# Kernel optimization log

Measured on AMD Instinct MI355X. Metric: run time of the kernel, lower is better.

The kernel has to match this reference:

```python
import jax, jax.numpy as jnp
import numpy as np

B, S, L, H, N_ITEMS = 16, 20, 64, 768, 50000  # sessions, max items/session, tokens/item, hidden, catalog
T = S * L
TEMP = 0.05       # config.temp
PAD_POS = 50      # pad item position id (see torch code)
EPS = 1e-8        # torch CosineSimilarity eps


def setup_inputs() -> dict:
    key = jax.random.key(0)
    k1, k2, k3, k4 = jax.random.split(key, 4)
    hidden = jax.random.normal(k1, (B, T, H), jnp.float32)
    emb = jax.random.normal(k2, (N_ITEMS, H), jnp.float32)
    # item position ids: each item's L tokens share position 1..S; padded items -> 50
    pos = np.tile(np.repeat(np.arange(1, S + 1), L)[None, :], (B, 1))  # [B,T]
    sess_len = np.asarray(jax.random.randint(k3, (B,), S // 2, S + 1))  # items per session
    item_idx = np.repeat(np.arange(S), L)[None, :]                      # [1,T]
    pos = np.where(item_idx < sess_len[:, None], pos, PAD_POS).astype(np.int32)
    attn = (pos != PAD_POS).astype(np.int32)
    attrs = np.asarray(jax.random.randint(k4, (B, T), 0, 4)).astype(np.int32)
    return {
        "hidden_states": hidden,
        "item_embedding": emb,
        "attention_mask": jnp.asarray(attn),
        "item_position_ids": jnp.asarray(pos),
        "attr_type_ids": jnp.asarray(attrs),
    }


def reference(hidden_states, item_embedding, attention_mask, item_position_ids, attr_type_ids):
    # --- RecformerPooler (pooler_type='item'): nan-mean pool tokens per item ---
    item_ids = jnp.arange(1, S + 1, dtype=item_position_ids.dtype)
    mask = item_position_ids[:, None, :] == item_ids[None, :, None]      # [B,S,T]
    counts = mask.sum(-1)                                                # [B,S]
    valid = counts > 0                                                   # items present in session
    maskf = mask.astype(hidden_states.dtype)
    pooled = jnp.einsum('bst,bth->bsh', maskf, hidden_states)
    pooled = pooled / jnp.maximum(counts, 1)[..., None].astype(hidden_states.dtype)
    # (torch produces NaN rows for invalid items; we carry `valid` instead)

    # --- Similarity: cosine / temp vs full item catalog ---
    pn = jnp.maximum(jnp.linalg.norm(pooled, axis=-1, keepdims=True), EPS)
    en = jnp.maximum(jnp.linalg.norm(item_embedding, axis=-1, keepdims=True), EPS)
    sim = jnp.einsum('bsh,nh->bns', pooled / pn, item_embedding / en) / TEMP  # [B,N,S]

    # --- reduce_session('maxsim'): NaN -> -inf, max over session items ---
    sim = jnp.where(valid[:, None, :], sim, -jnp.inf)
    scores = sim.max(axis=-1)  # [B, N]; trailing mean over attr dim (size 1) is identity
    return scores
```

## Files before the change

### kernel.cpp

```cpp
#include <hip/hip_runtime.h>

#define B_ 16
#define S_ 20
#define L_ 64
#define T_ 1280
#define H_ 768
#define NITEMS 50000
#define TEMP 0.05f
#define EPSN 1e-8f

#define BM 320
#define BN 128
#define BK 32
#define NKT (H_ / BK)

typedef __attribute__((ext_vector_type(8))) short short8;
typedef __attribute__((ext_vector_type(4))) short short4v;
typedef __attribute__((ext_vector_type(4))) float f32x4;

__device__ __forceinline__ unsigned short f2bf(float f) {
    unsigned int u = __float_as_uint(f);
    u = u + 0x7FFFu + ((u >> 16) & 1u);
    return (unsigned short)(u >> 16);
}

typedef __attribute__((address_space(3))) void lds_void;
typedef const __attribute__((address_space(1))) void gbl_void;
__device__ __forceinline__ void load_lds16(const void* g, void* l) {
    __builtin_amdgcn_global_load_lds((gbl_void*)g, (lds_void*)l, 16, 0, 0);
}

__global__ __launch_bounds__(192) void pool_kernel(const float* __restrict__ hidden,
                                                   const int* __restrict__ pos,
                                                   unsigned short* __restrict__ A,
                                                   int* __restrict__ valid) {
    const int row = blockIdx.x;
    const int b = row / S_, s = row % S_;
    const int tid = threadIdx.x;

    __shared__ float wgt[L_];
    __shared__ int cntS;
    __shared__ float red[3];

    const int* pbase = pos + b * T_ + s * L_;
    if (tid < L_) {
        const int match = (pbase[tid] == s + 1) ? 1 : 0;
        unsigned long long bal = __ballot(match);
        wgt[tid] = match ? 1.0f : 0.0f;
        if (tid == 0) cntS = (int)__popcll(bal);
    }
    __syncthreads();

    const int cnt = cntS;
    const float inv = 1.0f / (float)(cnt > 0 ? cnt : 1);
    const float* hbase = hidden + ((size_t)b * T_ + (size_t)s * L_) * H_ + tid * 4;

    float a0 = 0.f, a1 = 0.f, a2 = 0.f, a3 = 0.f;
#pragma unroll 8
    for (int t = 0; t < L_; ++t) {
        const float w = wgt[t];
        const float4 v = *reinterpret_cast<const float4*>(hbase + (size_t)t * H_);
        a0 += w * v.x; a1 += w * v.y; a2 += w * v.z; a3 += w * v.w;
    }
    a0 *= inv; a1 *= inv; a2 *= inv; a3 *= inv;

    float ss = a0 * a0 + a1 * a1 + a2 * a2 + a3 * a3;
#pragma unroll
    for (int off = 32; off; off >>= 1) ss += __shfl_xor(ss, off, 64);
    const int wave = tid >> 6, lane = tid & 63;
    if (lane == 0) red[wave] = ss;
    __syncthreads();
    const float tot = red[0] + red[1] + red[2];
    const float scale = 1.0f / (fmaxf(sqrtf(tot), EPSN) * TEMP);

    short4v w4;
    w4[0] = (short)f2bf(a0 * scale);
    w4[1] = (short)f2bf(a1 * scale);
    w4[2] = (short)f2bf(a2 * scale);
    w4[3] = (short)f2bf(a3 * scale);
    const int slot = tid >> 1;
    const int slotSw = (slot & ~3) | ((slot & 3) ^ (row & 3));
    *reinterpret_cast<short4v*>(A + (size_t)row * H_ + slotSw * 8 + (tid & 1) * 4) = w4;
    if (tid == 0) valid[row] = (cnt > 0) ? 1 : 0;
}

__global__ __launch_bounds__(256, 2) void gemm_kernel(const float* __restrict__ emb,
                                                      const unsigned short* __restrict__ A,
                                                      const int* __restrict__ valid,
                                                      float* __restrict__ out) {
    const int n0 = blockIdx.x * BN;
    const int tid = threadIdx.x;
    const int wave = tid >> 6, lane = tid & 63, quad = lane >> 4, lq = lane & 15;

    __shared__ alignas(16) short As[2][BM * BK];
    __shared__ alignas(16) short Bs[2][BN * BK];
    __shared__ float sEn[BN];
    __shared__ int sMask[B_];

    if (tid < B_) {
        int m = 0;
        for (int s = 0; s < S_; ++s) m |= (valid[tid * S_ + s] ? 1 : 0) << s;
        sMask[tid] = m;
    }

    const unsigned short* aSrc = A + (size_t)(tid >> 2) * H_ + (tid & 3) * 8;
    const int brLoc = tid >> 1;
    int brGlb = n0 + brLoc;
    if (brGlb > NITEMS - 1) brGlb = NITEMS - 1;
    const float* bSrc = emb + (size_t)brGlb * H_ + (tid & 1) * 16;
    const int bw0 = brLoc * BK + ((((tid & 1) * 2) + 0) ^ (brLoc & 3)) * 8;
    const int bw1 = brLoc * BK + ((((tid & 1) * 2) + 1) ^ (brLoc & 3)) * 8;

    float rowSq = 0.f;

    {
        const float4 v0 = *reinterpret_cast<const float4*>(bSrc);
        const float4 v1 = *reinterpret_cast<const float4*>(bSrc + 4);
        const float4 v2 = *reinterpret_cast<const float4*>(bSrc + 8);
        const float4 v3 = *reinterpret_cast<const float4*>(bSrc + 12);
#pragma unroll
        for (int i = 0; i < 5; ++i)
            load_lds16(aSrc + i * 64 * H_, (char*)(&As[0][0]) + tid * 16 + i * 4096);
        rowSq += v0.x * v0.x + v0.y * v0.y + v0.z * v0.z + v0.w * v0.w;
        rowSq += v1.x * v1.x + v1.y * v1.y + v1.z * v1.z + v1.w * v1.w;
        rowSq += v2.x * v2.x + v2.y * v2.y + v2.z * v2.z + v2.w * v2.w;
        rowSq += v3.x * v3.x + v3.y * v3.y + v3.z * v3.z + v3.w * v3.w;
        short8 lo, hi;
        lo[0] = (short)f2bf(v0.x); lo[1] = (short)f2bf(v0.y);
        lo[2] = (short)f2bf(v0.z); lo[3] = (short)f2bf(v0.w);
        lo[4] = (short)f2bf(v1.x); lo[5] = (short)f2bf(v1.y);
        lo[6] = (short)f2bf(v1.z); lo[7] = (short)f2bf(v1.w);
        hi[0] = (short)f2bf(v2.x); hi[1] = (short)f2bf(v2.y);
        hi[2] = (short)f2bf(v2.z); hi[3] = (short)f2bf(v2.w);
        hi[4] = (short)f2bf(v3.x); hi[5] = (short)f2bf(v3.y);
        hi[6] = (short)f2bf(v3.z); hi[7] = (short)f2bf(v3.w);
        *reinterpret_cast<short8*>(&Bs[0][bw0]) = lo;
        *reinterpret_cast<short8*>(&Bs[0][bw1]) = hi;
    }

    f32x4 acc[5][8];
#pragma unroll
    for (int i = 0; i < 5; ++i)
#pragma unroll
        for (int j = 0; j < 8; ++j) acc[i][j] = (f32x4)0.f;

    __syncthreads();

    int cur = 0;
    for (int kt = 0; kt < NKT; ++kt) {
        float4 v0, v1, v2, v3;
        const bool more = (kt + 1 < NKT);
        if (more) {
            const int k0 = (kt + 1) * BK;
            v0 = *reinterpret_cast<const float4*>(bSrc + k0);
            v1 = *reinterpret_cast<const float4*>(bSrc + k0 + 4);
            v2 = *reinterpret_cast<const float4*>(bSrc + k0 + 8);
            v3 = *reinterpret_cast<const float4*>(bSrc + k0 + 12);
#pragma unroll
            for (int i = 0; i < 5; ++i)
                load_lds16(aSrc + k0 + i * 64 * H_,
                           (char*)(&As[cur ^ 1][0]) + tid * 16 + i * 4096);
        }

        short8 bF[8];
#pragma unroll
        for (int nf = 0; nf < 8; ++nf) {
            const int rB = nf * 16 + lq;
            bF[nf] = *reinterpret_cast<const short8*>(
                &Bs[cur][rB * BK + ((quad ^ (lq & 3)) * 8)]);
        }

#pragma unroll
        for (int mf = 0; mf < 5; ++mf) {
            const int rA = wave * 80 + mf * 16 + lq;
            const short8 aF = *reinterpret_cast<const short8*>(
                &As[cur][rA * BK + ((quad ^ (lq & 3)) * 8)]);
#pragma unroll
            for (int nf = 0; nf < 8; ++nf)
                acc[mf][nf] =
                    __builtin_amdgcn_mfma_f32_16x16x32_bf16(aF, bF[nf], acc[mf][nf], 0, 0, 0);
        }

        if (more) {
            rowSq += v0.x * v0.x + v0.y * v0.y + v0.z * v0.z + v0.w * v0.w;
            rowSq += v1.x * v1.x + v1.y * v1.y + v1.z * v1.z + v1.w * v1.w;
            rowSq += v2.x * v2.x + v2.y * v2.y + v2.z * v2.z + v2.w * v2.w;
            rowSq += v3.x * v3.x + v3.y * v3.y + v3.z * v3.z + v3.w * v3.w;
            short8 lo, hi;
            lo[0] = (short)f2bf(v0.x); lo[1] = (short)f2bf(v0.y);
            lo[2] = (short)f2bf(v0.z); lo[3] = (short)f2bf(v0.w);
            lo[4] = (short)f2bf(v1.x); lo[5] = (short)f2bf(v1.y);
            lo[6] = (short)f2bf(v1.z); lo[7] = (short)f2bf(v1.w);
            hi[0] = (short)f2bf(v2.x); hi[1] = (short)f2bf(v2.y);
            hi[2] = (short)f2bf(v2.z); hi[3] = (short)f2bf(v2.w);
            hi[4] = (short)f2bf(v3.x); hi[5] = (short)f2bf(v3.y);
            hi[6] = (short)f2bf(v3.z); hi[7] = (short)f2bf(v3.w);
            *reinterpret_cast<short8*>(&Bs[cur ^ 1][bw0]) = lo;
            *reinterpret_cast<short8*>(&Bs[cur ^ 1][bw1]) = hi;
        }
        __syncthreads();
        cur ^= 1;
    }

    rowSq += __shfl_xor(rowSq, 1, 64);
    if (!(tid & 1)) sEn[brLoc] = fmaxf(sqrtf(rowSq), EPSN);
    __syncthreads();

#pragma unroll
    for (int nf = 0; nf < 8; ++nf) {
        const int ncol = nf * 16 + lq;
        const int n = n0 + ncol;
        const float inv_en = 1.0f / sEn[ncol];
#pragma unroll
        for (int bl = 0; bl < 4; ++bl) {
            const int bb = wave * 4 + bl;
            const int msk = sMask[bb];
            const int rLo = bl * S_;
            float lm = -__builtin_inff();
            const int mfLo = rLo >> 4;
            const int mfHi = (rLo + S_ - 1) >> 4;
#pragma unroll
            for (int mf = mfLo; mf <= mfHi; ++mf)
#pragma unroll
                for (int e = 0; e < 4; ++e) {
                    const int r = mf * 16 + quad * 4 + e;
                    const unsigned off = (unsigned)(r - rLo);
                    const bool ok = (off < (unsigned)S_) && ((msk >> off) & 1);
                    lm = ok ? fmaxf(lm, acc[mf][nf][e]) : lm;
                }
            lm = fmaxf(lm, __shfl_xor(lm, 16, 64));
            lm = fmaxf(lm, __shfl_xor(lm, 32, 64));
            if (quad == 0 && n < NITEMS)
                out[(size_t)bb * NITEMS + n] = lm * inv_en;
        }
    }
}

extern "C" void kernel_launch(void* const* d_in, const int* in_sizes, int n_in,
                              void* d_out, int out_size, void* d_ws, size_t ws_size,
                              hipStream_t stream) {
    const float* hidden = (const float*)d_in[0];
    const float* emb    = (const float*)d_in[1];
    const int*   pos    = (const int*)d_in[3];
    float* out = (float*)d_out;

    unsigned short* Abf = (unsigned short*)d_ws;
    int* valid = (int*)((char*)d_ws + (size_t)320 * 768 * 2);

    pool_kernel<<<dim3(320), dim3(192), 0, stream>>>(hidden, pos, Abf, valid);
    gemm_kernel<<<dim3((NITEMS + BN - 1) / BN), dim3(256), 0, stream>>>(emb, Abf, valid, out);
}
```

Before: 295.5 us.

## Rework GEMM LDS swizzle, move barrier before async loads, widen pool kernel

The GEMM main loop now uses one barrier per K-step, placed before the async global-to-LDS A loads are issued, with explicit vmcnt waits in place of the trailing __syncthreads. This aims to overlap the next tile's loads with the MFMA work and cut barrier stalls. The LDS XOR swizzle changes from row&3 to (row>>1)&3 for both A and B, with matching changes to the pool kernel's output layout, to reduce bank conflicts for the 16-lane fragment reads. The pool kernel moves to 384 threads with float2 loads. The manual waitcnt ordering is fragile and may cause races if the counts are wrong.

```diff
diff --git a/kernel.cpp b/kernel.cpp
--- a/kernel.cpp
+++ b/kernel.cpp
@@ -30,7 +30,7 @@
     __builtin_amdgcn_global_load_lds((gbl_void*)g, (lds_void*)l, 16, 0, 0);
 }
 
-__global__ __launch_bounds__(192) void pool_kernel(const float* __restrict__ hidden,
+__global__ __launch_bounds__(384) void pool_kernel(const float* __restrict__ hidden,
                                                    const int* __restrict__ pos,
                                                    unsigned short* __restrict__ A,
                                                    int* __restrict__ valid) {
@@ -40,7 +40,7 @@
 
     __shared__ float wgt[L_];
     __shared__ int cntS;
-    __shared__ float red[3];
+    __shared__ float red[6];
 
     const int* pbase = pos + b * T_ + s * L_;
     if (tid < L_) {
@@ -53,34 +53,34 @@
 
     const int cnt = cntS;
     const float inv = 1.0f / (float)(cnt > 0 ? cnt : 1);
-    const float* hbase = hidden + ((size_t)b * T_ + (size_t)s * L_) * H_ + tid * 4;
-
-    float a0 = 0.f, a1 = 0.f, a2 = 0.f, a3 = 0.f;
+    const float* hbase = hidden + ((size_t)b * T_ + (size_t)s * L_) * H_ + tid * 2;
+
+    float a0 = 0.f, a1 = 0.f;
 #pragma unroll 8
     for (int t = 0; t < L_; ++t) {
         const float w = wgt[t];
-        const float4 v = *reinterpret_cast<const float4*>(hbase + (size_t)t * H_);
-        a0 += w * v.x; a1 += w * v.y; a2 += w * v.z; a3 += w * v.w;
-    }
-    a0 *= inv; a1 *= inv; a2 *= inv; a3 *= inv;
-
-    float ss = a0 * a0 + a1 * a1 + a2 * a2 + a3 * a3;
+        const float2 v = *reinterpret_cast<const float2*>(hbase + (size_t)t * H_);
+        a0 += w * v.x; a1 += w * v.y;
+    }
+    a0 *= inv; a1 *= inv;
+
+    float ss = a0 * a0 + a1 * a1;
 #pragma unroll
     for (int off = 32; off; off >>= 1) ss += __shfl_xor(ss, off, 64);
     const int wave = tid >> 6, lane = tid & 63;
     if (lane == 0) red[wave] = ss;
     __syncthreads();
-    const float tot = red[0] + red[1] + red[2];
+    const float tot = red[0] + red[1] + red[2] + red[3] + red[4] + red[5];
     const float scale = 1.0f / (fmaxf(sqrtf(tot), EPSN) * TEMP);
 
-    short4v w4;
-    w4[0] = (short)f2bf(a0 * scale);
-    w4[1] = (short)f2bf(a1 * scale);
-    w4[2] = (short)f2bf(a2 * scale);
-    w4[3] = (short)f2bf(a3 * scale);
-    const int slot = tid >> 1;
-    const int slotSw = (slot & ~3) | ((slot & 3) ^ (row & 3));
-    *reinterpret_cast<short4v*>(A + (size_t)row * H_ + slotSw * 8 + (tid & 1) * 4) = w4;
+    const int chunk = tid >> 4;
+    const int cSlot = (tid >> 2) & 3;
+    const int phys = cSlot ^ ((row >> 1) & 3);
+    unsigned short r0 = f2bf(a0 * scale);
+    unsigned short r1 = f2bf(a1 * scale);
+    unsigned int pk = (unsigned int)r0 | ((unsigned int)r1 << 16);
+    *reinterpret_cast<unsigned int*>(A + (size_t)row * H_ + chunk * 32 + phys * 8 +
+                                     ((tid * 2) & 7)) = pk;
     if (tid == 0) valid[row] = (cnt > 0) ? 1 : 0;
 }
 
@@ -108,8 +108,9 @@
     int brGlb = n0 + brLoc;
     if (brGlb > NITEMS - 1) brGlb = NITEMS - 1;
     const float* bSrc = emb + (size_t)brGlb * H_ + (tid & 1) * 16;
-    const int bw0 = brLoc * BK + ((((tid & 1) * 2) + 0) ^ (brLoc & 3)) * 8;
-    const int bw1 = brLoc * BK + ((((tid & 1) * 2) + 1) ^ (brLoc & 3)) * 8;
+    const int bswz = (brLoc >> 1) & 3;
+    const int bw0 = brLoc * BK + ((((tid & 1) * 2) + 0) ^ bswz) * 8;
+    const int bw1 = brLoc * BK + ((((tid & 1) * 2) + 1) ^ bswz) * 8;
 
     float rowSq = 0.f;
 
@@ -137,6 +138,8 @@
         *reinterpret_cast<short8*>(&Bs[0][bw0]) = lo;
         *reinterpret_cast<short8*>(&Bs[0][bw1]) = hi;
     }
+    asm volatile("s_waitcnt vmcnt(0)" ::: "memory");
+    __syncthreads();
 
     f32x4 acc[5][8];
 #pragma unroll
@@ -144,43 +147,47 @@
 #pragma unroll
         for (int j = 0; j < 8; ++j) acc[i][j] = (f32x4)0.f;
 
-    __syncthreads();
-
+    const int fswz = (lq >> 1) & 3;
     int cur = 0;
     for (int kt = 0; kt < NKT; ++kt) {
+        const bool more = (kt + 1 < NKT);
         float4 v0, v1, v2, v3;
-        const bool more = (kt + 1 < NKT);
         if (more) {
             const int k0 = (kt + 1) * BK;
             v0 = *reinterpret_cast<const float4*>(bSrc + k0);
             v1 = *reinterpret_cast<const float4*>(bSrc + k0 + 4);
             v2 = *reinterpret_cast<const float4*>(bSrc + k0 + 8);
             v3 = *reinterpret_cast<const float4*>(bSrc + k0 + 12);
+        }
+        if (more) asm volatile("s_waitcnt vmcnt(4)" ::: "memory");
+        else      asm volatile("s_waitcnt vmcnt(0)" ::: "memory");
+        __builtin_amdgcn_s_barrier();
+        __builtin_amdgcn_sched_barrier(0);
+        asm volatile("" ::: "memory");
+        if (more) {
+            const int k0 = (kt + 1) * BK;
 #pragma unroll
             for (int i = 0; i < 5; ++i)
                 load_lds16(aSrc + k0 + i * 64 * H_,
                            (char*)(&As[cur ^ 1][0]) + tid * 16 + i * 4096);
         }
-
         short8 bF[8];
 #pragma unroll
         for (int nf = 0; nf < 8; ++nf) {
             const int rB = nf * 16 + lq;
             bF[nf] = *reinterpret_cast<const short8*>(
-                &Bs[cur][rB * BK + ((quad ^ (lq & 3)) * 8)]);
-        }
-
+                &Bs[cur][rB * BK + ((quad ^ fswz) * 8)]);
+        }
 #pragma unroll
         for (int mf = 0; mf < 5; ++mf) {
             const int rA = wave * 80 + mf * 16 + lq;
             const short8 aF = *reinterpret_cast<const short8*>(
-                &As[cur][rA * BK + ((quad ^ (lq & 3)) * 8)]);
+                &As[cur][rA * BK + ((quad ^ fswz) * 8)]);
 #pragma unroll
             for (int nf = 0; nf < 8; ++nf)
                 acc[mf][nf] =
                     __builtin_amdgcn_mfma_f32_16x16x32_bf16(aF, bF[nf], acc[mf][nf], 0, 0, 0);
         }
-
         if (more) {
             rowSq += v0.x * v0.x + v0.y * v0.y + v0.z * v0.z + v0.w * v0.w;
             rowSq += v1.x * v1.x + v1.y * v1.y + v1.z * v1.z + v1.w * v1.w;
@@ -198,7 +205,7 @@
             *reinterpret_cast<short8*>(&Bs[cur ^ 1][bw0]) = lo;
             *reinterpret_cast<short8*>(&Bs[cur ^ 1][bw1]) = hi;
         }
-        __syncthreads();
+        asm volatile("s_waitcnt lgkmcnt(0)" ::: "memory");
         cur ^= 1;
     }
 
@@ -247,6 +254,6 @@
     unsigned short* Abf = (unsigned short*)d_ws;
     int* valid = (int*)((char*)d_ws + (size_t)320 * 768 * 2);
 
-    pool_kernel<<<dim3(320), dim3(192), 0, stream>>>(hidden, pos, Abf, valid);
+    pool_kernel<<<dim3(320), dim3(384), 0, stream>>>(hidden, pos, Abf, valid);
     gemm_kernel<<<dim3((NITEMS + BN - 1) / BN), dim3(256), 0, stream>>>(emb, Abf, valid, out);
 }
```

Measured after the change: 295.3 us. No clear change (-0.1%).
